# Kernel tuning notes

Measured on AMD Instinct MI355X. Metric: run time of the kernel, lower is better.

Reference implementation:

```python
import jax, jax.numpy as jnp
import numpy as np

B, N, P, C = 2, 1024, 32, 256   # batch, num queries, in_points, eff_in_dim(=in_dim, G=1)
OP = 32                          # out_points
HID = 128                        # parameter_generator hidden width
TOTAL = C * C + OP * P           # channel + spatial mixing params per query


def setup_inputs() -> dict:
    key = jax.random.key(0)
    ks = jax.random.split(key, 8)
    sc = lambda k, shape, s=0.02: jax.random.normal(k, shape, jnp.float32) * s
    return {
        "x": jax.random.normal(ks[0], (B, N, 1, P, C), jnp.float32),
        "query": jax.random.normal(ks[1], (B, N, C), jnp.float32),
        # LayerNorm initialized unit-norm style (gamma * width**-0.5), bias zero
        "ln_w": jnp.full((C,), C ** -0.5, jnp.float32),
        "ln_b": jnp.zeros((C,), jnp.float32),
        "w1": sc(ks[2], (HID, C)),
        "b1": jnp.zeros((HID,), jnp.float32),
        "w2": sc(ks[3], (TOTAL, HID)),
        "b2": sc(ks[4], (TOTAL,), 0.05),
        "m_beta": jnp.zeros((C,), jnp.float32),
        "s_beta": jnp.zeros((OP,), jnp.float32),
        "proj_w": sc(ks[5], (C, OP * C)),
        "proj_b": jnp.zeros((C,), jnp.float32),
    }


def reference(x, query, ln_w, ln_b, w1, b1, w2, b2, m_beta, s_beta, proj_w, proj_b):
    # parameter_generator: LayerNorm(eps=1e-6) -> Linear(C,128) -> Linear(128,TOTAL)
    mu = jnp.mean(query, axis=-1, keepdims=True)
    var = jnp.var(query, axis=-1, keepdims=True)  # biased, matches torch LayerNorm
    q = (query - mu) * jax.lax.rsqrt(var + 1e-6) * ln_w + ln_b
    h = q @ w1.T + b1                               # [B,N,128]
    params = h @ w2.T + b2                          # [B,N,TOTAL]

    cm = params[..., : C * C].reshape(B, N, C, C)   # channel mixing [B,N,Cin,Cout]
    sm = params[..., C * C :].reshape(B, N, OP, P)  # spatial mixing [B,N,OP,P]

    xs = x[:, :, 0]                                 # [B,N,P,C] (g==1)
    # baddbmm(channel_bias, x, channel_mixing) then GELU (exact erf)
    out = jnp.einsum('bnpc,bncd->bnpd', xs, cm) + m_beta
    out = jax.nn.gelu(out, approximate=False)
    # baddbmm(spatial_bias, spatial_mixing, out) then GELU
    out = jnp.einsum('bnop,bnpd->bnod', sm, out) + s_beta[None, None, :, None]
    out = jax.nn.gelu(out, approximate=False)

    out = out.reshape(B, N, OP * C) @ proj_w.T + proj_b  # tuo_proj -> [B,N,C]
    return out
```

## Files before the change

### kernel.cpp

```cpp
#include <hip/hip_runtime.h>
#include <hip/hip_bf16.h>

#define TKN   2048
#define CDIM  256
#define PDIM  32
#define ODIM  32
#define HIDD  128
#define CCSZ  65536
#define TOTSZ 66560
#define KSPL  16

typedef unsigned short u16;
typedef __bf16 bf16x8 __attribute__((ext_vector_type(8)));
typedef float f32x4 __attribute__((ext_vector_type(4)));
typedef unsigned short u16x4 __attribute__((ext_vector_type(4)));
typedef unsigned short u16x8 __attribute__((ext_vector_type(8)));

__device__ __forceinline__ u16 f2b(float f){
  __hip_bfloat16 h = __float2bfloat16(f);
  return *reinterpret_cast<u16*>(&h);
}
__device__ __forceinline__ float gelu_exact(float x){
  return 0.5f * x * (1.0f + erff(x * 0.70710678118654752f));
}
__device__ __forceinline__ void gload16(const void* g, void* l){
  __builtin_amdgcn_global_load_lds(
      (const __attribute__((address_space(1))) unsigned int*)g,
      (__attribute__((address_space(3))) unsigned int*)l, 16, 0, 0);
}

__global__ __launch_bounds__(256) void k_prep_h(
    const float* __restrict__ query, const float* __restrict__ ln_w,
    const float* __restrict__ ln_b, const float* __restrict__ w1,
    const float* __restrict__ b1, u16* __restrict__ H){
  const int t = blockIdx.x;
  const int tid = threadIdx.x;
  __shared__ float qs[CDIM];
  __shared__ float red[8];
  __shared__ float stat[2];
  float v = query[(size_t)t*CDIM + tid];
  float s = v, s2 = v*v;
  #pragma unroll
  for(int o=32;o>0;o>>=1){ s += __shfl_down(s,o,64); s2 += __shfl_down(s2,o,64); }
  const int wv = tid>>6;
  if((tid&63)==0){ red[wv]=s; red[4+wv]=s2; }
  __syncthreads();
  if(tid==0){
    float ss=red[0]+red[1]+red[2]+red[3];
    float qq=red[4]+red[5]+red[6]+red[7];
    float mu=ss/(float)CDIM;
    float var=qq/(float)CDIM - mu*mu;
    stat[0]=mu; stat[1]=rsqrtf(var+1e-6f);
  }
  __syncthreads();
  qs[tid] = (v - stat[0])*stat[1]*ln_w[tid] + ln_b[tid];
  __syncthreads();
  if(tid < HIDD){
    const float* wr = w1 + (size_t)tid*CDIM;
    float acc = b1[tid];
    #pragma unroll 8
    for(int c=0;c<CDIM;c++) acc += qs[c]*wr[c];
    H[(size_t)t*HIDD + tid] = f2b(acc);
  }
}

__global__ __launch_bounds__(256) void k_prep_w2(
    const float* __restrict__ w2, const float* __restrict__ b2,
    u16* __restrict__ w2s, float* __restrict__ b2p){
  const int gid = blockIdx.x*256 + threadIdx.x;
  const int dst = gid >> 4;
  const int ch  = gid & 15;
  if(dst >= TOTSZ) return;
  const int j = (dst < CCSZ) ? (((dst & 255) << 8) | (dst >> 8)) : dst;
  const float* src = w2 + (size_t)j*HIDD + ch*8;
  u16* o = w2s + (size_t)dst*HIDD + (size_t)((ch ^ (dst & 7))*8);
  u16x8 tv;
  #pragma unroll
  for(int i=0;i<8;i++) tv[i] = f2b(src[i]);
  *(u16x8*)o = tv;
  if(ch == 0) b2p[dst] = b2[j];
}

__global__ __launch_bounds__(256) void k_prep_pw(
    const float* __restrict__ pw, u16* __restrict__ pwb){
  const int gid = blockIdx.x*256 + threadIdx.x;
  const float* s = pw + (size_t)gid*8;
  u16x8 tv;
  #pragma unroll
  for(int i=0;i<8;i++) tv[i] = f2b(s[i]);
  *(u16x8*)(pwb + (size_t)gid*8) = tv;
}

__global__ __launch_bounds__(256, 3) void k_params(
    const u16* __restrict__ H, const u16* __restrict__ w2s,
    const float* __restrict__ b2p, u16* __restrict__ pbuf,
    int msteps, int chnk){
  __shared__ __align__(16) u16 S[4][32][72];
  const int tid = threadIdx.x;
  const int lane = tid & 63;
  const int w = tid >> 6;
  const int n0 = blockIdx.x * 128;
  const int tbase = blockIdx.y * (chnk >> 1);
  const int wmi = w >> 1, wni = w & 1;
  const int r15 = lane & 15, g = lane >> 4;
  bf16x8 bfr[4][4];
  #pragma unroll
  for(int ks=0;ks<4;ks++)
    #pragma unroll
    for(int nt=0;nt<4;nt++){
      const int rr = wni*64 + nt*16 + r15;
      const int pc = (ks*4 + g) ^ (rr & 7);
      bfr[ks][nt] = *(const bf16x8*)(w2s + (size_t)(n0+rr)*HIDD + pc*8);
    }
  float b2v[4];
  #pragma unroll
  for(int nt=0;nt<4;nt++) b2v[nt] = b2p[n0 + wni*64 + nt*16 + r15];
  const int jrow = lane >> 3, jc8 = lane & 7;
  for(int m=0; m<msteps; m++){
    const int t0 = tbase + m*64 + wmi*32;
    bf16x8 afr[2][4];
    #pragma unroll
    for(int mt=0;mt<2;mt++){
      const u16* ap = H + (size_t)(t0 + mt*16 + r15)*HIDD + g*8;
      #pragma unroll
      for(int ks=0;ks<4;ks++) afr[mt][ks] = *(const bf16x8*)(ap + ks*32);
    }
    f32x4 acc[2][4] = {};
    #pragma unroll
    for(int ks=0;ks<4;ks++)
      #pragma unroll
      for(int mt=0;mt<2;mt++)
        #pragma unroll
        for(int nt=0;nt<4;nt++)
          acc[mt][nt] = __builtin_amdgcn_mfma_f32_16x16x32_bf16(afr[mt][ks], bfr[ks][nt], acc[mt][nt], 0,0,0);
    #pragma unroll
    for(int mt=0;mt<2;mt++)
      #pragma unroll
      for(int nt=0;nt<4;nt++)
        #pragma unroll
        for(int r=0;r<4;r++)
          S[w][mt*16 + g*4 + r][nt*16 + r15] = f2b(acc[mt][nt][r] + b2v[nt]);
    u16* dst = pbuf + ((size_t)blockIdx.x*chnk + t0)*128 + wni*64;
    #pragma unroll
    for(int j=0;j<4;j++){
      const int lt = j*8 + jrow;
      *(u16x8*)(dst + (size_t)lt*128 + jc8*8) = *(const u16x8*)&S[w][lt][jc8*8];
    }
  }
}

__global__ __launch_bounds__(256) void k_token(
    const float* __restrict__ xg, const u16* __restrict__ pbuf,
    const float* __restrict__ m_beta, const float* __restrict__ s_beta,
    u16* __restrict__ out2, int chnk){
  __shared__ u16 xs[PDIM][264];
  __shared__ u16 smt[ODIM][40];
  __shared__ u16 o1[128][40];
  const int tl = blockIdx.x;
  const int dh = blockIdx.y;
  const int tid = threadIdx.x;
  const int lane = tid & 63;
  const int w = tid >> 6;
  const int r15 = lane & 15, g = lane >> 4;
  const size_t prow = (size_t)chnk*128;

  {
    const f32x4* src = (const f32x4*)(xg + (size_t)tl*8192);
    #pragma unroll
    for(int i=0;i<8;i++){
      f32x4 v = src[tid + 256*i];
      const int flat = (tid + 256*i)*4;
      const int p = flat >> 8, c = flat & 255;
      u16x4 t4; t4[0]=f2b(v[0]); t4[1]=f2b(v[1]); t4[2]=f2b(v[2]); t4[3]=f2b(v[3]);
      *(u16x4*)&xs[p][c] = t4;
    }
  }
  if(tid < 128){
    const u16* s = pbuf + ((size_t)(512 + (tid>>4)))*prow + (size_t)tl*128 + (tid&15)*8;
    const int o = (tid*8) >> 5, p = (tid*8) & 31;
    *(u16x8*)&smt[o][p] = *(const u16x8*)s;
  }
  __syncthreads();

  f32x4 acc[2][2] = {};
  const u16* cbase = pbuf + (size_t)(dh*128)*2*prow + (size_t)tl*128;
  #pragma unroll
  for(int ks=0;ks<8;ks++){
    bf16x8 af[2], bf[2];
    #pragma unroll
    for(int mt=0;mt<2;mt++){
      const int dloc = w*32 + mt*16 + r15;
      af[mt] = *(const bf16x8*)(cbase + (size_t)dloc*2*prow + (size_t)(ks>>2)*prow + (ks&3)*32 + g*8);
    }
    #pragma unroll
    for(int nt=0;nt<2;nt++){
      const int p = nt*16 + r15;
      bf[nt] = *(const bf16x8*)&xs[p][ks*32 + g*8];
    }
    #pragma unroll
    for(int mt=0;mt<2;mt++)
      #pragma unroll
      for(int nt=0;nt<2;nt++)
        acc[mt][nt] = __builtin_amdgcn_mfma_f32_16x16x32_bf16(af[mt], bf[nt], acc[mt][nt], 0,0,0);
  }
  #pragma unroll
  for(int mt=0;mt<2;mt++){
    const int d0 = w*32 + mt*16 + g*4;
    const f32x4 mb = *(const f32x4*)&m_beta[dh*128 + d0];
    #pragma unroll
    for(int nt=0;nt<2;nt++){
      const int p = nt*16 + r15;
      #pragma unroll
      for(int r=0;r<4;r++)
        o1[d0+r][p] = f2b(gelu_exact(acc[mt][nt][r] + mb[r]));
    }
  }
  __syncthreads();

  f32x4 acc2[2][2] = {};
  {
    bf16x8 af[2], bf2[2];
    #pragma unroll
    for(int mt=0;mt<2;mt++){
      const int dloc = w*32 + mt*16 + r15;
      af[mt] = *(const bf16x8*)&o1[dloc][g*8];
    }
    #pragma unroll
    for(int nt=0;nt<2;nt++){
      const int o = nt*16 + r15;
      bf2[nt] = *(const bf16x8*)&smt[o][g*8];
    }
    #pragma unroll
    for(int mt=0;mt<2;mt++)
      #pragma unroll
      for(int nt=0;nt<2;nt++)
        acc2[mt][nt] = __builtin_amdgcn_mfma_f32_16x16x32_bf16(af[mt], bf2[nt], acc2[mt][nt], 0,0,0);
  }
  u16 (*o2t)[264] = xs;
  #pragma unroll
  for(int nt=0;nt<2;nt++){
    const int o = nt*16 + r15;
    const float sb = s_beta[o];
    #pragma unroll
    for(int mt=0;mt<2;mt++){
      const int d0 = w*32 + mt*16 + g*4;
      u16x4 t4;
      #pragma unroll
      for(int r=0;r<4;r++) t4[r] = f2b(gelu_exact(acc2[mt][nt][r] + sb));
      *(u16x4*)&o2t[o][d0] = t4;
    }
  }
  __syncthreads();
  {
    u16* dst = out2 + (size_t)tl*8192 + dh*128;
    #pragma unroll
    for(int i=0;i<2;i++){
      const int flat = (i*256 + tid)*8;
      const int o = flat >> 7, dd = flat & 127;
      *(u16x8*)(dst + o*256 + dd) = *(const u16x8*)&o2t[o][dd];
    }
  }
}

__global__ __launch_bounds__(512) void k_proj(
    const u16* __restrict__ out2, const u16* __restrict__ pwb,
    float* __restrict__ part){
  __shared__ u16 Ab[2][64*32];
  __shared__ u16 Bb[2][256*32];
  const int tid = threadIdx.x;
  const int lane = tid & 63, w = tid >> 6;
  const int r15 = lane & 15, g = lane >> 4;
  const int m0 = blockIdx.x * 64;
  const int k0 = blockIdx.y * 512;
  const int wm = (w >> 2) * 32;
  const int wn = (w & 3) * 64;
  const int srow = lane >> 2;
  const int cs   = lane & 3;
  const int a_row = (w & 3)*16 + srow;
  const u16* a_src = out2 + (size_t)(m0 + a_row)*8192 + k0 + (size_t)((cs ^ (a_row & 3))*8);
  const int b_row0 = (2*w)*16 + srow;
  const int b_row1 = (2*w+1)*16 + srow;
  const u16* b_src0 = pwb + (size_t)b_row0*8192 + k0 + (size_t)((cs ^ (b_row0 & 3))*8);
  const u16* b_src1 = pwb + (size_t)b_row1*8192 + k0 + (size_t)((cs ^ (b_row1 & 3))*8);

  f32x4 acc[2][4] = {};

  #define STAGE(buf, kt) do{                                         \
    const int ko = (kt)*32;                                          \
    if(w < 4) gload16(a_src + ko, (char*)&Ab[buf][0] + w*1024);      \
    gload16(b_src0 + ko, (char*)&Bb[buf][0] + (2*w)*1024);           \
    gload16(b_src1 + ko, (char*)&Bb[buf][0] + (2*w+1)*1024);         \
  }while(0)

  STAGE(0, 0);
  __syncthreads();
  int cur = 0;
  for(int kt=0; kt<16; kt++){
    if(kt < 15){ STAGE(cur^1, kt+1); }
    bf16x8 af[2], bf[4];
    #pragma unroll
    for(int mt=0;mt<2;mt++){
      const int row = wm + mt*16 + r15;
      af[mt] = *(const bf16x8*)((char*)&Ab[cur][0] + row*64 + ((g ^ (row&3))*16));
    }
    #pragma unroll
    for(int nt=0;nt<4;nt++){
      const int row = wn + nt*16 + r15;
      bf[nt] = *(const bf16x8*)((char*)&Bb[cur][0] + row*64 + ((g ^ (row&3))*16));
    }
    #pragma unroll
    for(int mt=0;mt<2;mt++)
      #pragma unroll
      for(int nt=0;nt<4;nt++)
        acc[mt][nt] = __builtin_amdgcn_mfma_f32_16x16x32_bf16(af[mt], bf[nt], acc[mt][nt], 0,0,0);
    __syncthreads();
    cur ^= 1;
  }
  #undef STAGE

  float* pbase = part + (size_t)blockIdx.y*TKN*CDIM;
  #pragma unroll
  for(int mt=0;mt<2;mt++)
    #pragma unroll
    for(int nt=0;nt<4;nt++){
      const int t = m0 + wm + mt*16 + g*4;
      const int e = wn + nt*16 + r15;
      #pragma unroll
      for(int r=0;r<4;r++)
        pbase[(size_t)(t+r)*CDIM + e] = acc[mt][nt][r];
    }
}

__global__ __launch_bounds__(256) void k_combine(
    const float* __restrict__ part, const float* __restrict__ pb,
    float* __restrict__ out){
  const int i4 = blockIdx.x*256 + threadIdx.x;
  const int e4 = (i4 & 63)*4;
  f32x4 s = *(const f32x4*)&pb[e4];
  #pragma unroll
  for(int z=0;z<KSPL;z++) s += *(const f32x4*)&part[(size_t)z*524288 + (size_t)i4*4];
  *(f32x4*)&out[(size_t)i4*4] = s;
}

extern "C" void kernel_launch(void* const* d_in, const int* in_sizes, int n_in,
                              void* d_out, int out_size, void* d_ws, size_t ws_size,
                              hipStream_t stream){
  const float* x     = (const float*)d_in[0];
  const float* query = (const float*)d_in[1];
  const float* ln_w  = (const float*)d_in[2];
  const float* ln_b  = (const float*)d_in[3];
  const float* w1    = (const float*)d_in[4];
  const float* b1    = (const float*)d_in[5];
  const float* w2    = (const float*)d_in[6];
  const float* b2    = (const float*)d_in[7];
  const float* m_beta= (const float*)d_in[8];
  const float* s_beta= (const float*)d_in[9];
  const float* pw    = (const float*)d_in[10];
  const float* pb    = (const float*)d_in[11];
  float* out = (float*)d_out;
  char* ws = (char*)d_ws;

  const size_t need_big = 192u*1024u*1024u;
  const int chnk = (ws_size >= need_big) ? 1024 : 256;
  const int nch  = TKN / chnk;

  size_t off = 0;
  u16* H     = (u16*)(ws + off);  off += (size_t)TKN*HIDD*2;
  u16* w2s   = (u16*)(ws + off);  off += (size_t)TOTSZ*HIDD*2;
  float* b2p = (float*)(ws + off);off += (size_t)TOTSZ*4;
  u16* pwb   = (u16*)(ws + off);  off += (size_t)CDIM*8192*2;
  u16* pbuf  = (u16*)(ws + off);  off += (size_t)chnk*TOTSZ*2;
  u16* out2  = (u16*)(ws + off);  off += (size_t)TKN*8192*2;
  float* part= (float*)pbuf;

  k_prep_h<<<TKN, 256, 0, stream>>>(query, ln_w, ln_b, w1, b1, H);
  k_prep_w2<<<4160, 256, 0, stream>>>(w2, b2, w2s, b2p);
  k_prep_pw<<<1024, 256, 0, stream>>>(pw, pwb);
  for(int ch=0; ch<nch; ch++){
    k_params<<<dim3(520,2), 256, 0, stream>>>(H + (size_t)ch*chnk*HIDD, w2s, b2p, pbuf,
                                              chnk/128, chnk);
    k_token<<<dim3(chnk,2), 256, 0, stream>>>(x + (size_t)ch*chnk*8192, pbuf, m_beta, s_beta,
                                              out2 + (size_t)ch*chnk*8192, chnk);
  }
  k_proj<<<dim3(32,KSPL), 512, 0, stream>>>(out2, pwb, part);
  k_combine<<<512, 256, 0, stream>>>(part, pb, out);
}
```

Measured before the change: 256.2 us.

## Store generated params token-major in MFMA fragment order; one block per token

The weight-prep permutation now orders channel-mixing columns so that each token's generated parameters land in pbuf token-major, already in MFMA A-fragment order. k_token can then read each fragment with a contiguous 16-byte per-lane load instead of strided gathers across a chunk-wide row. k_token now covers all 256 output channels in one 512-thread block instead of two 256-thread blocks, so x is staged once per token. k_params gets a fixed two-step loop, a 2D grid over tokens and a higher occupancy hint. Writes from k_params now stride by TOTSZ per token, which may make stores less coalesced, and the higher occupancy hint may add register pressure.

```diff
diff --git a/kernel.cpp b/kernel.cpp
--- a/kernel.cpp
+++ b/kernel.cpp
@@ -22,11 +22,6 @@
 }
 __device__ __forceinline__ float gelu_exact(float x){
   return 0.5f * x * (1.0f + erff(x * 0.70710678118654752f));
-}
-__device__ __forceinline__ void gload16(const void* g, void* l){
-  __builtin_amdgcn_global_load_lds(
-      (const __attribute__((address_space(1))) unsigned int*)g,
-      (__attribute__((address_space(3))) unsigned int*)l, 16, 0, 0);
 }
 
 __global__ __launch_bounds__(256) void k_prep_h(
@@ -68,17 +63,26 @@
     const float* __restrict__ w2, const float* __restrict__ b2,
     u16* __restrict__ w2s, float* __restrict__ b2p){
   const int gid = blockIdx.x*256 + threadIdx.x;
-  const int dst = gid >> 4;
-  const int ch  = gid & 15;
-  if(dst >= TOTSZ) return;
-  const int j = (dst < CCSZ) ? (((dst & 255) << 8) | (dst >> 8)) : dst;
+  const int n  = gid >> 4;
+  const int ch = gid & 15;
+  if(n >= TOTSZ) return;
+  int j;
+  if(n < CCSZ){
+    const int Tidx = n >> 9, within = n & 511;
+    const int g = within >> 7, r = (within >> 3) & 15, e = within & 7;
+    const int d = (Tidx >> 3)*16 + r;
+    const int c = (Tidx & 7)*32 + g*8 + e;
+    j = c*256 + d;
+  } else {
+    j = n;
+  }
   const float* src = w2 + (size_t)j*HIDD + ch*8;
-  u16* o = w2s + (size_t)dst*HIDD + (size_t)((ch ^ (dst & 7))*8);
+  u16* o = w2s + (size_t)n*HIDD + (size_t)((ch ^ (n & 7))*8);
   u16x8 tv;
   #pragma unroll
   for(int i=0;i<8;i++) tv[i] = f2b(src[i]);
   *(u16x8*)o = tv;
-  if(ch == 0) b2p[dst] = b2[j];
+  if(ch == 0) b2p[n] = b2[j];
 }
 
 __global__ __launch_bounds__(256) void k_prep_pw(
@@ -91,16 +95,15 @@
   *(u16x8*)(pwb + (size_t)gid*8) = tv;
 }
 
-__global__ __launch_bounds__(256, 3) void k_params(
+__global__ __launch_bounds__(256, 6) void k_params(
     const u16* __restrict__ H, const u16* __restrict__ w2s,
-    const float* __restrict__ b2p, u16* __restrict__ pbuf,
-    int msteps, int chnk){
+    const float* __restrict__ b2p, u16* __restrict__ pbuf){
   __shared__ __align__(16) u16 S[4][32][72];
   const int tid = threadIdx.x;
   const int lane = tid & 63;
   const int w = tid >> 6;
   const int n0 = blockIdx.x * 128;
-  const int tbase = blockIdx.y * (chnk >> 1);
+  const int tbase = blockIdx.y * 128;
   const int wmi = w >> 1, wni = w & 1;
   const int r15 = lane & 15, g = lane >> 4;
   bf16x8 bfr[4][4];
@@ -116,7 +119,8 @@
   #pragma unroll
   for(int nt=0;nt<4;nt++) b2v[nt] = b2p[n0 + wni*64 + nt*16 + r15];
   const int jrow = lane >> 3, jc8 = lane & 7;
-  for(int m=0; m<msteps; m++){
+  #pragma unroll
+  for(int m=0; m<2; m++){
     const int t0 = tbase + m*64 + wmi*32;
     bf16x8 afr[2][4];
     #pragma unroll
@@ -140,58 +144,55 @@
         #pragma unroll
         for(int r=0;r<4;r++)
           S[w][mt*16 + g*4 + r][nt*16 + r15] = f2b(acc[mt][nt][r] + b2v[nt]);
-    u16* dst = pbuf + ((size_t)blockIdx.x*chnk + t0)*128 + wni*64;
+    u16* dst = pbuf + (size_t)t0*TOTSZ + n0 + wni*64;
     #pragma unroll
     for(int j=0;j<4;j++){
       const int lt = j*8 + jrow;
-      *(u16x8*)(dst + (size_t)lt*128 + jc8*8) = *(const u16x8*)&S[w][lt][jc8*8];
-    }
-  }
-}
-
-__global__ __launch_bounds__(256) void k_token(
+      *(u16x8*)(dst + (size_t)lt*TOTSZ + jc8*8) = *(const u16x8*)&S[w][lt][jc8*8];
+    }
+  }
+}
+
+__global__ __launch_bounds__(512, 8) void k_token(
     const float* __restrict__ xg, const u16* __restrict__ pbuf,
     const float* __restrict__ m_beta, const float* __restrict__ s_beta,
-    u16* __restrict__ out2, int chnk){
+    u16* __restrict__ out2){
   __shared__ u16 xs[PDIM][264];
   __shared__ u16 smt[ODIM][40];
-  __shared__ u16 o1[128][40];
+  __shared__ u16 o1[CDIM][40];
   const int tl = blockIdx.x;
-  const int dh = blockIdx.y;
   const int tid = threadIdx.x;
   const int lane = tid & 63;
   const int w = tid >> 6;
   const int r15 = lane & 15, g = lane >> 4;
-  const size_t prow = (size_t)chnk*128;
+  const u16* tok = pbuf + (size_t)tl*TOTSZ;
 
   {
     const f32x4* src = (const f32x4*)(xg + (size_t)tl*8192);
     #pragma unroll
-    for(int i=0;i<8;i++){
-      f32x4 v = src[tid + 256*i];
-      const int flat = (tid + 256*i)*4;
+    for(int i=0;i<4;i++){
+      const int idx = tid + 512*i;
+      f32x4 v = src[idx];
+      const int flat = idx*4;
       const int p = flat >> 8, c = flat & 255;
       u16x4 t4; t4[0]=f2b(v[0]); t4[1]=f2b(v[1]); t4[2]=f2b(v[2]); t4[3]=f2b(v[3]);
       *(u16x4*)&xs[p][c] = t4;
     }
   }
   if(tid < 128){
-    const u16* s = pbuf + ((size_t)(512 + (tid>>4)))*prow + (size_t)tl*128 + (tid&15)*8;
+    const u16* s = tok + CCSZ + tid*8;
     const int o = (tid*8) >> 5, p = (tid*8) & 31;
     *(u16x8*)&smt[o][p] = *(const u16x8*)s;
   }
   __syncthreads();
 
   f32x4 acc[2][2] = {};
-  const u16* cbase = pbuf + (size_t)(dh*128)*2*prow + (size_t)tl*128;
   #pragma unroll
   for(int ks=0;ks<8;ks++){
     bf16x8 af[2], bf[2];
     #pragma unroll
-    for(int mt=0;mt<2;mt++){
-      const int dloc = w*32 + mt*16 + r15;
-      af[mt] = *(const bf16x8*)(cbase + (size_t)dloc*2*prow + (size_t)(ks>>2)*prow + (ks&3)*32 + g*8);
-    }
+    for(int mt=0;mt<2;mt++)
+      af[mt] = *(const bf16x8*)(tok + (size_t)(((w*2+mt)*8 + ks)*512) + lane*8);
     #pragma unroll
     for(int nt=0;nt<2;nt++){
       const int p = nt*16 + r15;
@@ -206,7 +207,7 @@
   #pragma unroll
   for(int mt=0;mt<2;mt++){
     const int d0 = w*32 + mt*16 + g*4;
-    const f32x4 mb = *(const f32x4*)&m_beta[dh*128 + d0];
+    const f32x4 mb = *(const f32x4*)&m_beta[d0];
     #pragma unroll
     for(int nt=0;nt<2;nt++){
       const int p = nt*16 + r15;
@@ -222,8 +223,8 @@
     bf16x8 af[2], bf2[2];
     #pragma unroll
     for(int mt=0;mt<2;mt++){
-      const int dloc = w*32 + mt*16 + r15;
-      af[mt] = *(const bf16x8*)&o1[dloc][g*8];
+      const int d = w*32 + mt*16 + r15;
+      af[mt] = *(const bf16x8*)&o1[d][g*8];
     }
     #pragma unroll
     for(int nt=0;nt<2;nt++){
@@ -252,12 +253,12 @@
   }
   __syncthreads();
   {
-    u16* dst = out2 + (size_t)tl*8192 + dh*128;
+    u16* dst = out2 + (size_t)tl*8192;
     #pragma unroll
     for(int i=0;i<2;i++){
-      const int flat = (i*256 + tid)*8;
-      const int o = flat >> 7, dd = flat & 127;
-      *(u16x8*)(dst + o*256 + dd) = *(const u16x8*)&o2t[o][dd];
+      const int flat = (i*512 + tid)*8;
+      const int o = flat >> 8, dd = flat & 255;
+      *(u16x8*)(dst + flat) = *(const u16x8*)&o2t[o][dd];
     }
   }
 }
@@ -285,11 +286,14 @@
 
   f32x4 acc[2][4] = {};
 
+  #define GL16(gp, lp) __builtin_amdgcn_global_load_lds( \
+      (const __attribute__((address_space(1))) unsigned int*)(gp), \
+      (__attribute__((address_space(3))) unsigned int*)(lp), 16, 0, 0)
   #define STAGE(buf, kt) do{                                         \
     const int ko = (kt)*32;                                          \
-    if(w < 4) gload16(a_src + ko, (char*)&Ab[buf][0] + w*1024);      \
-    gload16(b_src0 + ko, (char*)&Bb[buf][0] + (2*w)*1024);           \
-    gload16(b_src1 + ko, (char*)&Bb[buf][0] + (2*w+1)*1024);         \
+    if(w < 4) GL16(a_src + ko, (char*)&Ab[buf][0] + w*1024);         \
+    GL16(b_src0 + ko, (char*)&Bb[buf][0] + (2*w)*1024);              \
+    GL16(b_src1 + ko, (char*)&Bb[buf][0] + (2*w+1)*1024);            \
   }while(0)
 
   STAGE(0, 0);
@@ -317,6 +321,7 @@
     cur ^= 1;
   }
   #undef STAGE
+  #undef GL16
 
   float* pbase = part + (size_t)blockIdx.y*TKN*CDIM;
   #pragma unroll
@@ -377,10 +382,9 @@
   k_prep_w2<<<4160, 256, 0, stream>>>(w2, b2, w2s, b2p);
   k_prep_pw<<<1024, 256, 0, stream>>>(pw, pwb);
   for(int ch=0; ch<nch; ch++){
-    k_params<<<dim3(520,2), 256, 0, stream>>>(H + (size_t)ch*chnk*HIDD, w2s, b2p, pbuf,
-                                              chnk/128, chnk);
-    k_token<<<dim3(chnk,2), 256, 0, stream>>>(x + (size_t)ch*chnk*8192, pbuf, m_beta, s_beta,
-                                              out2 + (size_t)ch*chnk*8192, chnk);
+    k_params<<<dim3(520, chnk/128), 256, 0, stream>>>(H + (size_t)ch*chnk*HIDD, w2s, b2p, pbuf);
+    k_token<<<chnk, 512, 0, stream>>>(x + (size_t)ch*chnk*8192, pbuf, m_beta, s_beta,
+                                      out2 + (size_t)ch*chnk*8192);
   }
   k_proj<<<dim3(32,KSPL), 512, 0, stream>>>(out2, pwb, part);
   k_combine<<<512, 256, 0, stream>>>(part, pb, out);
```

New measurement: 530.5 us. 2.07x slower.
